# Performance work log

Hardware: AMD Instinct MI355X
Metric: run time of the kernel (lower is better)

## Reference

```python
import jax, jax.numpy as jnp
import numpy as np

EMBED, MID = 2048, 256
SLOPE = 0.2

def _lrelu(v):
    return jnp.where(v >= 0, v, SLOPE * v)

def setup_inputs() -> dict:
    key = jax.random.key(0)
    ks = jax.random.split(key, 9)
    B, C, L = 4, EMBED, 4096
    s_in = 1.0 / np.sqrt(C)
    s_mid = 1.0 / np.sqrt(MID)
    return {
        "x":   jax.random.normal(ks[0], (B, C, L), dtype=jnp.float32),
        "W_t": jax.random.uniform(ks[1], (MID, C), jnp.float32, -s_in, s_in),
        "b_t": jax.random.uniform(ks[2], (MID,), jnp.float32, -s_in, s_in),
        "W_p": jax.random.uniform(ks[3], (MID, C), jnp.float32, -s_in, s_in),
        "b_p": jax.random.uniform(ks[4], (MID,), jnp.float32, -s_in, s_in),
        "W_g": jax.random.uniform(ks[5], (MID, C), jnp.float32, -s_in, s_in),
        "b_g": jax.random.uniform(ks[6], (MID,), jnp.float32, -s_in, s_in),
        "W_o": jax.random.uniform(ks[7], (C, MID), jnp.float32, -s_mid, s_mid),
        "b_o": jax.random.uniform(ks[8], (C,), jnp.float32, -s_mid, s_mid),
    }

def reference(x, W_t, b_t, W_p, b_p, W_g, b_g, W_o, b_o):
    # x: [B, C, L]; 1x1 conv == channel matmul. Dropout is identity (eval mode).
    theta = _lrelu(jnp.einsum('mc,bcl->bml', W_t, x) + b_t[None, :, None])  # [B, M, L]
    phi   = _lrelu(jnp.einsum('mc,bcl->bml', W_p, x) + b_p[None, :, None])  # [B, M, L]
    gamma = _lrelu(jnp.einsum('mc,bcl->bml', W_g, x) + b_g[None, :, None])  # [B, M, L]
    # scores: phi^T @ theta -> [B, L, L], fixed scale 1/32
    scores = jnp.einsum('bmi,bmj->bij', phi, theta) / 32.0
    attn = jax.nn.softmax(scores, axis=-1)
    # y: attn @ gamma^T -> [B, L, M], then back to [B, M, L]
    y = jnp.einsum('bij,bmj->bmi', attn, gamma)
    out = x + _lrelu(jnp.einsum('cm,bml->bcl', W_o, y) + b_o[None, :, None])
    return out
```

## Files before the change

kernel.cpp:

```cpp
#include <hip/hip_runtime.h>
#include <stdint.h>

#define B_ 4
#define C_ 2048
#define L_ 4096
#define M_ 256
#define M3_ 768
#define SLOPE_ 0.2f
#define SPLIT_ 4
#define KVB_ 32

typedef __attribute__((ext_vector_type(8))) short short8;
typedef __attribute__((ext_vector_type(4))) float f32x4;

__device__ __forceinline__ unsigned short f2bf(float f) {
    union { float f; unsigned u; } v; v.f = f;
    unsigned r = v.u + 0x7FFF + ((v.u >> 16) & 1);
    return (unsigned short)(r >> 16);
}
__device__ __forceinline__ unsigned short f2bf_rz(float f) {
    union { float f; unsigned u; } v; v.f = f;
    return (unsigned short)(v.u >> 16);
}
__device__ __forceinline__ unsigned pack2(float a, float b) {
    return (unsigned)f2bf(a) | ((unsigned)f2bf(b) << 16);
}
__device__ __forceinline__ float lrelu(float v) { return v >= 0.f ? v : SLOPE_ * v; }

__device__ __forceinline__ void gload_lds16(const void* g, void* l) {
    __builtin_amdgcn_global_load_lds(
        (const __attribute__((address_space(1))) void*)g,
        (__attribute__((address_space(3))) void*)l, 16, 0, 0);
}

__global__ __launch_bounds__(256) void prep_x(
    const float* __restrict__ x, unsigned short* __restrict__ xT)
{
    const int l = blockIdx.x * 64 + (threadIdx.x & 63);
    const int c = blockIdx.y * 32 + (threadIdx.x >> 6) * 8;
    const int b = blockIdx.z;
    const float* src = x + ((size_t)b * C_ + c) * L_ + l;
    unsigned v[4];
    #pragma unroll
    for (int j = 0; j < 4; ++j)
        v[j] = pack2(src[(size_t)(2 * j) * L_], src[(size_t)(2 * j + 1) * L_]);
    *reinterpret_cast<uint4*>(&xT[((size_t)b * L_ + l) * C_ + c]) =
        *reinterpret_cast<uint4*>(v);
}

__global__ __launch_bounds__(256) void prep_w(
    const float* __restrict__ Wt, const float* __restrict__ Wp,
    const float* __restrict__ Wg, const float* __restrict__ Wo,
    unsigned short* __restrict__ w3, unsigned short* __restrict__ wo)
{
    const size_t NW = (size_t)M_ * C_;
    size_t e = ((size_t)blockIdx.x * 256 + threadIdx.x) * 8;
    const float* src; unsigned short* dst;
    if (e < NW)          { src = Wt + e;          dst = w3 + e; }
    else if (e < 2 * NW) { src = Wp + (e - NW);   dst = w3 + e; }
    else if (e < 3 * NW) { src = Wg + (e - 2*NW); dst = w3 + e; }
    else                 { src = Wo + (e - 3*NW); dst = wo + (e - 3*NW); }
    float4 a = *reinterpret_cast<const float4*>(src);
    float4 b = *reinterpret_cast<const float4*>(src + 4);
    unsigned v[4] = { pack2(a.x, a.y), pack2(a.z, a.w),
                      pack2(b.x, b.y), pack2(b.z, b.w) };
    *reinterpret_cast<uint4*>(dst) = *reinterpret_cast<uint4*>(v);
}

__global__ __launch_bounds__(256) void proj_kernel(
    const unsigned short* __restrict__ w3,
    const float* __restrict__ bt, const float* __restrict__ bp,
    const float* __restrict__ bg,
    const unsigned short* __restrict__ xT,
    unsigned short* __restrict__ theta,
    unsigned short* __restrict__ phi,
    unsigned short* __restrict__ gammaT)
{
    __shared__ unsigned short As[2][128 * 64];
    __shared__ unsigned short Bs[2][128 * 64];

    const int l0 = blockIdx.x * 128;
    const int m0 = blockIdx.y * 128;
    const int b  = blockIdx.z;
    const int t  = threadIdx.x;
    const int wave = t >> 6, lane = t & 63;
    const int lr = lane & 15, lg = lane >> 4;
    const int wm = (wave >> 1) * 64, wl = (wave & 1) * 64;

    const int which = m0 >> 8;
    const float* bsrc = (which == 0) ? bt : (which == 1) ? bp : bg;
    const int mw = m0 & 255;

    const unsigned short* abase = w3 + (size_t)m0 * C_;
    const unsigned short* bbase = xT + ((size_t)b * L_ + l0) * C_;

    const int srow = lane >> 3;
    const int scol = ((lane & 7) ^ srow) * 8;

    auto stage = [&](unsigned short* A, unsigned short* Bb, int k0) {
        #pragma unroll
        for (int i = 0; i < 4; ++i) {
            int chunk = wave * 4 + i;
            int row = chunk * 8 + srow;
            gload_lds16(abase + (size_t)row * C_ + k0 + scol, A + chunk * 512);
            gload_lds16(bbase + (size_t)row * C_ + k0 + scol, Bb + chunk * 512);
        }
    };

    f32x4 acc[4][4] = {};

    stage(As[0], Bs[0], 0);
    __syncthreads();

    int cur = 0;
    for (int k0 = 0; k0 < C_; k0 += 64) {
        if (k0 + 64 < C_) stage(As[cur ^ 1], Bs[cur ^ 1], k0 + 64);

        #pragma unroll
        for (int ks = 0; ks < 2; ++ks) {
            short8 af[4], bf[4];
            #pragma unroll
            for (int mi = 0; mi < 4; ++mi)
                af[mi] = *reinterpret_cast<const short8*>(
                    &As[cur][(wm + mi * 16 + lr) * 64 +
                             ((ks * 32 + lg * 8) ^ ((lr & 7) << 3))]);
            #pragma unroll
            for (int ni = 0; ni < 4; ++ni)
                bf[ni] = *reinterpret_cast<const short8*>(
                    &Bs[cur][(wl + ni * 16 + lr) * 64 +
                             ((ks * 32 + lg * 8) ^ ((lr & 7) << 3))]);
            #pragma unroll
            for (int mi = 0; mi < 4; ++mi)
                #pragma unroll
                for (int ni = 0; ni < 4; ++ni)
                    acc[mi][ni] = __builtin_amdgcn_mfma_f32_16x16x32_bf16(
                        af[mi], bf[ni], acc[mi][ni], 0, 0, 0);
        }
        __syncthreads();
        cur ^= 1;
    }

    if (which < 2) {
        unsigned short* dst = (which == 0) ? theta : phi;
        const float scale = (which == 1) ? 0.03125f : 1.0f;
        #pragma unroll
        for (int mi = 0; mi < 4; ++mi) {
            const int mloc = mw + wm + mi * 16 + lg * 4;
            float b0 = bsrc[mloc], b1 = bsrc[mloc + 1];
            float b2 = bsrc[mloc + 2], b3 = bsrc[mloc + 3];
            #pragma unroll
            for (int ni = 0; ni < 4; ++ni) {
                int l = l0 + wl + ni * 16 + lr;
                uint2 pk;
                pk.x = pack2(lrelu(acc[mi][ni][0] + b0) * scale,
                             lrelu(acc[mi][ni][1] + b1) * scale);
                pk.y = pack2(lrelu(acc[mi][ni][2] + b2) * scale,
                             lrelu(acc[mi][ni][3] + b3) * scale);
                *reinterpret_cast<uint2*>(&dst[((size_t)b * L_ + l) * M_ + mloc]) = pk;
            }
        }
    } else {
        #pragma unroll
        for (int mi = 0; mi < 4; ++mi) {
            #pragma unroll
            for (int r = 0; r < 4; ++r) {
                int m = mw + wm + mi * 16 + lg * 4 + r;
                float bias = bsrc[m];
                #pragma unroll
                for (int ni = 0; ni < 4; ++ni) {
                    int l = l0 + wl + ni * 16 + lr;
                    gammaT[((size_t)b * M_ + m) * L_ + l] =
                        f2bf(lrelu(acc[mi][ni][r] + bias));
                }
            }
        }
    }
}

__global__ __launch_bounds__(512, 1) void attn_kernel(
    const unsigned short* __restrict__ phi,
    const unsigned short* __restrict__ theta,
    const unsigned short* __restrict__ gammaT,
    float* __restrict__ yp,
    float* __restrict__ rsp)
{
    __shared__ unsigned short Ks[2][KVB_ * 256];
    __shared__ unsigned short Vs[2][256 * KVB_];
    __shared__ unsigned short Ps[8][32][42];

    const int q0 = blockIdx.x * 256;
    const int s  = blockIdx.y;
    const int b  = blockIdx.z;
    const int kvbase = s * (L_ / SPLIT_);
    const int t  = threadIdx.x;
    const int wave = t >> 6, lane = t & 63;
    const int lr = lane & 15, lg = lane >> 4;

    const unsigned short* theta_b = theta  + (size_t)b * L_ * M_;
    const unsigned short* gamma_b = gammaT + (size_t)b * M_ * L_;

    short8 qf[2][8];
    #pragma unroll
    for (int u = 0; u < 2; ++u) {
        const unsigned short* qrow =
            phi + ((size_t)b * L_ + q0 + wave * 32 + u * 16 + lr) * M_ + lg * 8;
        #pragma unroll
        for (int ks = 0; ks < 8; ++ks)
            qf[u][ks] = *reinterpret_cast<const short8*>(qrow + ks * 32);
    }

    f32x4 accy[2][16] = {};
    float rsum[2][4] = {};

    auto stage_k = [&](unsigned short* buf, int kv0) {
        #pragma unroll
        for (int q = 0; q < 2; ++q) {
            int c   = q * 512 + t;
            int row = c >> 5;
            int cb  = (c & 31) << 4;
            int cbs = cb ^ ((row & 7) << 4);
            const unsigned short* src = theta_b + (size_t)(kv0 + row) * M_ + (cbs >> 1);
            unsigned short* ldst = buf + ((size_t)(q * 512 + wave * 64) << 3);
            gload_lds16(src, ldst);
        }
    };
    auto stage_v = [&](unsigned short* buf, int kv0) {
        #pragma unroll
        for (int q = 0; q < 2; ++q) {
            int c  = q * 512 + t;
            int mh = c >> 3;
            int tb = ((c & 7) << 4) ^ ((mh & 7) << 4);
            int m  = mh * 2 + (tb >> 6);
            int j  = (tb & 63) >> 1;
            const unsigned short* src = gamma_b + (size_t)m * L_ + kv0 + j;
            unsigned short* ldst = buf + ((size_t)(q * 512 + wave * 64) << 3);
            gload_lds16(src, ldst);
        }
    };

    stage_k(&Ks[0][0], kvbase);
    stage_v(&Vs[0][0], kvbase);
    __syncthreads();

    int cur = 0;
    for (int it = 0; it < L_ / SPLIT_ / KVB_; ++it) {
        if (it + 1 < L_ / SPLIT_ / KVB_) {
            stage_k(&Ks[cur ^ 1][0], kvbase + (it + 1) * KVB_);
            stage_v(&Vs[cur ^ 1][0], kvbase + (it + 1) * KVB_);
        }

        f32x4 sacc[2][2] = {};
        __builtin_amdgcn_s_setprio(1);
        #pragma unroll
        for (int ks = 0; ks < 8; ++ks) {
            #pragma unroll
            for (int jt = 0; jt < 2; ++jt) {
                int jr = jt * 16 + lr;
                int cbl = ks * 64 + lg * 16;
                short8 bf = *reinterpret_cast<const short8*>(
                    &Ks[cur][jr * 256 + (((cbl ^ ((jr & 7) << 4)) >> 1))]);
                sacc[0][jt] = __builtin_amdgcn_mfma_f32_16x16x32_bf16(qf[0][ks], bf, sacc[0][jt], 0, 0, 0);
                sacc[1][jt] = __builtin_amdgcn_mfma_f32_16x16x32_bf16(qf[1][ks], bf, sacc[1][jt], 0, 0, 0);
            }
        }
        __builtin_amdgcn_s_setprio(0);

        #pragma unroll
        for (int u = 0; u < 2; ++u)
            #pragma unroll
            for (int jt = 0; jt < 2; ++jt)
                #pragma unroll
                for (int r = 0; r < 4; ++r) {
                    float p = __expf(sacc[u][jt][r]);
                    rsum[u][r] += p;
                    Ps[wave][u * 16 + lg * 4 + r][lr + 16 * jt] = f2bf_rz(p);
                }

        short8 paf[2];
        paf[0] = *reinterpret_cast<const short8*>(&Ps[wave][lr][lg * 8]);
        paf[1] = *reinterpret_cast<const short8*>(&Ps[wave][16 + lr][lg * 8]);
        __builtin_amdgcn_s_setprio(1);
        #pragma unroll
        for (int mt = 0; mt < 16; ++mt) {
            int m = mt * 16 + lr;
            int byte = (m >> 1) * 128 +
                       ((((m & 1) * 64 + lg * 16)) ^ (((m >> 1) & 7) << 4));
            short8 bf = *reinterpret_cast<const short8*>(&Vs[cur][byte >> 1]);
            accy[0][mt] = __builtin_amdgcn_mfma_f32_16x16x32_bf16(paf[0], bf, accy[0][mt], 0, 0, 0);
            accy[1][mt] = __builtin_amdgcn_mfma_f32_16x16x32_bf16(paf[1], bf, accy[1][mt], 0, 0, 0);
        }
        __builtin_amdgcn_s_setprio(0);

        __syncthreads();
        cur ^= 1;
    }

    float* ypb = yp + (((size_t)(s * B_ + b) * L_) + q0) * M_;
    #pragma unroll
    for (int u = 0; u < 2; ++u)
        #pragma unroll
        for (int r = 0; r < 4; ++r) {
            int row = wave * 32 + u * 16 + lg * 4 + r;
            #pragma unroll
            for (int mt = 0; mt < 16; ++mt)
                ypb[(size_t)row * M_ + lr + 16 * mt] = accy[u][mt][r];
            float ssum = rsum[u][r];
            #pragma unroll
            for (int off = 1; off < 16; off <<= 1)
                ssum += __shfl_xor(ssum, off, 64);
            if (lr == 0)
                rsp[((size_t)(s * B_ + b) * L_) + q0 + row] = ssum;
        }
}

__global__ __launch_bounds__(256) void reduce_kernel(
    const float* __restrict__ yp,
    const float* __restrict__ rsp,
    unsigned short* __restrict__ y)
{
    const int idx = blockIdx.x * 256 + threadIdx.x;
    const int ml  = (idx * 8) & (M_ - 1);
    const int row = (idx * 8) >> 8;
    const int b   = row >> 12;
    const int l   = row & (L_ - 1);

    float acc[8] = {};
    float rs = 0.f;
    #pragma unroll
    for (int s = 0; s < SPLIT_; ++s) {
        const float* p = yp + (((size_t)(s * B_ + b) * L_) + l) * M_ + ml;
        float4 a = *reinterpret_cast<const float4*>(p);
        float4 c = *reinterpret_cast<const float4*>(p + 4);
        acc[0] += a.x; acc[1] += a.y; acc[2] += a.z; acc[3] += a.w;
        acc[4] += c.x; acc[5] += c.y; acc[6] += c.z; acc[7] += c.w;
        rs += rsp[((size_t)(s * B_ + b) * L_) + l];
    }
    float inv = 1.f / rs;
    unsigned v[4] = { pack2(acc[0] * inv, acc[1] * inv),
                      pack2(acc[2] * inv, acc[3] * inv),
                      pack2(acc[4] * inv, acc[5] * inv),
                      pack2(acc[6] * inv, acc[7] * inv) };
    *reinterpret_cast<uint4*>(&y[((size_t)b * L_ + l) * M_ + ml]) =
        *reinterpret_cast<uint4*>(v);
}

__global__ __launch_bounds__(256) void out_kernel(
    const float* __restrict__ x,
    const unsigned short* __restrict__ wo,
    const float* __restrict__ bo,
    const unsigned short* __restrict__ y,
    float* __restrict__ out)
{
    __shared__ unsigned short As[2][128 * 64];
    __shared__ unsigned short Bs[2][128 * 64];

    const int l0 = blockIdx.x * 128;
    const int c0 = blockIdx.y * 128;
    const int b  = blockIdx.z;
    const int t  = threadIdx.x;
    const int wave = t >> 6, lane = t & 63;
    const int lr = lane & 15, lg = lane >> 4;
    const int wm = (wave >> 1) * 64, wl = (wave & 1) * 64;

    const unsigned short* abase = wo + (size_t)c0 * M_;
    const unsigned short* bbase = y + ((size_t)b * L_ + l0) * M_;

    const int srow = lane >> 3;
    const int scol = ((lane & 7) ^ srow) * 8;

    auto stage = [&](unsigned short* A, unsigned short* Bb, int k0) {
        #pragma unroll
        for (int i = 0; i < 4; ++i) {
            int chunk = wave * 4 + i;
            int row = chunk * 8 + srow;
            gload_lds16(abase + (size_t)row * M_ + k0 + scol, A + chunk * 512);
            gload_lds16(bbase + (size_t)row * M_ + k0 + scol, Bb + chunk * 512);
        }
    };

    f32x4 acc[4][4] = {};

    stage(As[0], Bs[0], 0);
    __syncthreads();

    int cur = 0;
    for (int k0 = 0; k0 < M_; k0 += 64) {
        if (k0 + 64 < M_) stage(As[cur ^ 1], Bs[cur ^ 1], k0 + 64);

        #pragma unroll
        for (int ks = 0; ks < 2; ++ks) {
            short8 af[4], bf[4];
            #pragma unroll
            for (int mi = 0; mi < 4; ++mi)
                af[mi] = *reinterpret_cast<const short8*>(
                    &As[cur][(wm + mi * 16 + lr) * 64 +
                             ((ks * 32 + lg * 8) ^ ((lr & 7) << 3))]);
            #pragma unroll
            for (int ni = 0; ni < 4; ++ni)
                bf[ni] = *reinterpret_cast<const short8*>(
                    &Bs[cur][(wl + ni * 16 + lr) * 64 +
                             ((ks * 32 + lg * 8) ^ ((lr & 7) << 3))]);
            #pragma unroll
            for (int mi = 0; mi < 4; ++mi)
                #pragma unroll
                for (int ni = 0; ni < 4; ++ni)
                    acc[mi][ni] = __builtin_amdgcn_mfma_f32_16x16x32_bf16(
                        af[mi], bf[ni], acc[mi][ni], 0, 0, 0);
        }
        __syncthreads();
        cur ^= 1;
    }

    #pragma unroll
    for (int mi = 0; mi < 4; ++mi) {
        #pragma unroll
        for (int r = 0; r < 4; ++r) {
            int c = c0 + wm + mi * 16 + lg * 4 + r;
            float bias = bo[c];
            #pragma unroll
            for (int ni = 0; ni < 4; ++ni) {
                int l = l0 + wl + ni * 16 + lr;
                size_t idx = ((size_t)b * C_ + c) * L_ + l;
                out[idx] = x[idx] + lrelu(acc[mi][ni][r] + bias);
            }
        }
    }
}

extern "C" void kernel_launch(void* const* d_in, const int* in_sizes, int n_in,
                              void* d_out, int out_size, void* d_ws, size_t ws_size,
                              hipStream_t stream) {
    const float* x  = (const float*)d_in[0];
    const float* Wt = (const float*)d_in[1];
    const float* bt = (const float*)d_in[2];
    const float* Wp = (const float*)d_in[3];
    const float* bp = (const float*)d_in[4];
    const float* Wg = (const float*)d_in[5];
    const float* bg = (const float*)d_in[6];
    const float* Wo = (const float*)d_in[7];
    const float* bo = (const float*)d_in[8];
    float* out = (float*)d_out;

    unsigned short* xT    = (unsigned short*)d_ws;
    unsigned short* w3    = xT + (size_t)B_ * L_ * C_;
    unsigned short* wob   = w3 + (size_t)M3_ * C_;
    unsigned short* theta = wob + (size_t)C_ * M_;
    unsigned short* phi   = theta + (size_t)B_ * L_ * M_;
    unsigned short* gammaT= phi   + (size_t)B_ * L_ * M_;

    float* yp  = (float*)xT;
    float* rsp = (float*)w3;
    unsigned short* yb = theta;

    prep_x<<<dim3(L_ / 64, C_ / 32, B_), 256, 0, stream>>>(x, xT);
    prep_w<<<dim3(2097152 / 8 / 256), 256, 0, stream>>>(Wt, Wp, Wg, Wo, w3, wob);
    proj_kernel<<<dim3(L_ / 128, M3_ / 128, B_), 256, 0, stream>>>(
        w3, bt, bp, bg, xT, theta, phi, gammaT);
    attn_kernel<<<dim3(L_ / 256, SPLIT_, B_), 512, 0, stream>>>(
        phi, theta, gammaT, yp, rsp);
    reduce_kernel<<<dim3((B_ * L_ * M_ / 8) / 256), 256, 0, stream>>>(yp, rsp, yb);
    out_kernel<<<dim3(L_ / 128, C_ / 128, B_), 256, 0, stream>>>(x, wob, bo, yb, out);
}
```

Measured before the change: 279.3 us.

## Drop LDS double buffering in projection and output GEMMs to raise occupancy

Replaces the double-buffered LDS staging in proj_kernel and out_kernel with a single buffer that is loaded, synchronized and then consumed on each K step. It also adds a minimum of 3 blocks per CU to the launch bounds. This halves LDS use per block (64KB to 32KB) so more blocks fit per CU, relying on cross-block interleaving to hide global-load latency instead of in-block prefetch. In exchange each iteration now has two barriers and no overlap of loads with MFMA work inside a block, and the occupancy hint may constrain registers.

```diff
diff --git a/kernel.cpp b/kernel.cpp
--- a/kernel.cpp
+++ b/kernel.cpp
@@ -67,7 +67,7 @@
     *reinterpret_cast<uint4*>(dst) = *reinterpret_cast<uint4*>(v);
 }
 
-__global__ __launch_bounds__(256) void proj_kernel(
+__global__ __launch_bounds__(256, 3) void proj_kernel(
     const unsigned short* __restrict__ w3,
     const float* __restrict__ bt, const float* __restrict__ bp,
     const float* __restrict__ bg,
@@ -76,8 +76,8 @@
     unsigned short* __restrict__ phi,
     unsigned short* __restrict__ gammaT)
 {
-    __shared__ unsigned short As[2][128 * 64];
-    __shared__ unsigned short Bs[2][128 * 64];
+    __shared__ unsigned short As[128 * 64];
+    __shared__ unsigned short Bs[128 * 64];
 
     const int l0 = blockIdx.x * 128;
     const int m0 = blockIdx.y * 128;
@@ -97,24 +97,18 @@
     const int srow = lane >> 3;
     const int scol = ((lane & 7) ^ srow) * 8;
 
-    auto stage = [&](unsigned short* A, unsigned short* Bb, int k0) {
+    f32x4 acc[4][4] = {};
+
+    for (int k0 = 0; k0 < C_; k0 += 64) {
+        __syncthreads();
         #pragma unroll
         for (int i = 0; i < 4; ++i) {
             int chunk = wave * 4 + i;
             int row = chunk * 8 + srow;
-            gload_lds16(abase + (size_t)row * C_ + k0 + scol, A + chunk * 512);
-            gload_lds16(bbase + (size_t)row * C_ + k0 + scol, Bb + chunk * 512);
-        }
-    };
-
-    f32x4 acc[4][4] = {};
-
-    stage(As[0], Bs[0], 0);
-    __syncthreads();
-
-    int cur = 0;
-    for (int k0 = 0; k0 < C_; k0 += 64) {
-        if (k0 + 64 < C_) stage(As[cur ^ 1], Bs[cur ^ 1], k0 + 64);
+            gload_lds16(abase + (size_t)row * C_ + k0 + scol, As + chunk * 512);
+            gload_lds16(bbase + (size_t)row * C_ + k0 + scol, Bs + chunk * 512);
+        }
+        __syncthreads();
 
         #pragma unroll
         for (int ks = 0; ks < 2; ++ks) {
@@ -122,13 +116,13 @@
             #pragma unroll
             for (int mi = 0; mi < 4; ++mi)
                 af[mi] = *reinterpret_cast<const short8*>(
-                    &As[cur][(wm + mi * 16 + lr) * 64 +
-                             ((ks * 32 + lg * 8) ^ ((lr & 7) << 3))]);
+                    &As[(wm + mi * 16 + lr) * 64 +
+                        ((ks * 32 + lg * 8) ^ ((lr & 7) << 3))]);
             #pragma unroll
             for (int ni = 0; ni < 4; ++ni)
                 bf[ni] = *reinterpret_cast<const short8*>(
-                    &Bs[cur][(wl + ni * 16 + lr) * 64 +
-                             ((ks * 32 + lg * 8) ^ ((lr & 7) << 3))]);
+                    &Bs[(wl + ni * 16 + lr) * 64 +
+                        ((ks * 32 + lg * 8) ^ ((lr & 7) << 3))]);
             #pragma unroll
             for (int mi = 0; mi < 4; ++mi)
                 #pragma unroll
@@ -136,8 +130,6 @@
                     acc[mi][ni] = __builtin_amdgcn_mfma_f32_16x16x32_bf16(
                         af[mi], bf[ni], acc[mi][ni], 0, 0, 0);
         }
-        __syncthreads();
-        cur ^= 1;
     }
 
     if (which < 2) {
@@ -344,15 +336,15 @@
         *reinterpret_cast<uint4*>(v);
 }
 
-__global__ __launch_bounds__(256) void out_kernel(
+__global__ __launch_bounds__(256, 3) void out_kernel(
     const float* __restrict__ x,
     const unsigned short* __restrict__ wo,
     const float* __restrict__ bo,
     const unsigned short* __restrict__ y,
     float* __restrict__ out)
 {
-    __shared__ unsigned short As[2][128 * 64];
-    __shared__ unsigned short Bs[2][128 * 64];
+    __shared__ unsigned short As[128 * 64];
+    __shared__ unsigned short Bs[128 * 64];
 
     const int l0 = blockIdx.x * 128;
     const int c0 = blockIdx.y * 128;
@@ -368,24 +360,18 @@
     const int srow = lane >> 3;
     const int scol = ((lane & 7) ^ srow) * 8;
 
-    auto stage = [&](unsigned short* A, unsigned short* Bb, int k0) {
+    f32x4 acc[4][4] = {};
+
+    for (int k0 = 0; k0 < M_; k0 += 64) {
+        __syncthreads();
         #pragma unroll
         for (int i = 0; i < 4; ++i) {
             int chunk = wave * 4 + i;
             int row = chunk * 8 + srow;
-            gload_lds16(abase + (size_t)row * M_ + k0 + scol, A + chunk * 512);
-            gload_lds16(bbase + (size_t)row * M_ + k0 + scol, Bb + chunk * 512);
-        }
-    };
-
-    f32x4 acc[4][4] = {};
-
-    stage(As[0], Bs[0], 0);
-    __syncthreads();
-
-    int cur = 0;
-    for (int k0 = 0; k0 < M_; k0 += 64) {
-        if (k0 + 64 < M_) stage(As[cur ^ 1], Bs[cur ^ 1], k0 + 64);
+            gload_lds16(abase + (size_t)row * M_ + k0 + scol, As + chunk * 512);
+            gload_lds16(bbase + (size_t)row * M_ + k0 + scol, Bs + chunk * 512);
+        }
+        __syncthreads();
 
         #pragma unroll
         for (int ks = 0; ks < 2; ++ks) {
@@ -393,13 +379,13 @@
             #pragma unroll
             for (int mi = 0; mi < 4; ++mi)
                 af[mi] = *reinterpret_cast<const short8*>(
-                    &As[cur][(wm + mi * 16 + lr) * 64 +
-                             ((ks * 32 + lg * 8) ^ ((lr & 7) << 3))]);
+                    &As[(wm + mi * 16 + lr) * 64 +
+                        ((ks * 32 + lg * 8) ^ ((lr & 7) << 3))]);
             #pragma unroll
             for (int ni = 0; ni < 4; ++ni)
                 bf[ni] = *reinterpret_cast<const short8*>(
-                    &Bs[cur][(wl + ni * 16 + lr) * 64 +
-                             ((ks * 32 + lg * 8) ^ ((lr & 7) << 3))]);
+                    &Bs[(wl + ni * 16 + lr) * 64 +
+                        ((ks * 32 + lg * 8) ^ ((lr & 7) << 3))]);
             #pragma unroll
             for (int mi = 0; mi < 4; ++mi)
                 #pragma unroll
@@ -407,8 +393,6 @@
                     acc[mi][ni] = __builtin_amdgcn_mfma_f32_16x16x32_bf16(
                         af[mi], bf[ni], acc[mi][ni], 0, 0, 0);
         }
-        __syncthreads();
-        cur ^= 1;
     }
 
     #pragma unroll
```

Measured after the change: 269.5 us. 1.04x faster.
